# Kernel tuning notes

Hardware: AMD Instinct MI355X
Metric: run time of the kernel (lower is better)

The kernel has to match this reference:

```python
import math
import jax, jax.numpy as jnp
import numpy as np

N, E, D, B, S, H = 16384, 196608, 256, 256, 64, 8
DH = D // H
BN_INV = 1.0 / math.sqrt(1.0 + 1e-5)  # eval-mode BN: mean=0, var=1, eps=1e-5
LOG2 = math.log(2.0)


def _mlp(x, w1, b1, w2, b2):
    # Linear -> SiLU -> Linear
    return jax.nn.silu(x @ w1 + b1) @ w2 + b2


def _bn(x, g, b):
    # BatchNorm1d in eval mode with running_mean=0, running_var=1
    return x * (BN_INV * g) + b


def _graph_ln(x, g, b):
    # pyg LayerNorm(mode='graph') called with batch=None: normalize over all nodes+features
    mu = jnp.mean(x)
    xc = x - mu
    var = jnp.mean(xc * xc)
    return xc * jax.lax.rsqrt(var + 1e-5) * g + b


def _forward(x, edge_index, edge_attr,
             node_w1, node_b1, node_w2, node_b2,
             c_w1, c_b1, c_w2, c_b2,
             bn_e_g, bn_e_b, bn_h_g, bn_h_b,
             n1l_g, n1l_b, n1a_g, n1a_b, n2_g, n2_b,
             wq, bq, wk, bk, wv, bv, wo, bo,
             aff_w1, aff_b1, aff_w2, aff_b2,
             fn_g, fn_b, fc_w1, fc_b1, fc_w2, fc_b2):
    row, col = edge_index[0], edge_index[1]

    # ---- PotNetConvGate local branch ----
    # A, B, V, U MLPs (all take node features) computed with stacked weights [4,D,D]
    hid = jax.nn.silu(jnp.einsum('nd,kdf->knf', x, node_w1) + node_b1[:, None, :])
    node_out = jnp.einsum('knf,kfg->kng', hid, node_w2) + node_b2[:, None, :]
    h_A, h_B, h_V, h_U = node_out[0], node_out[1], node_out[2], node_out[3]
    e_C = _mlp(edge_attr, c_w1, c_b1, c_w2, c_b2)  # [E,D]

    score = jax.nn.relu(_bn(h_A[row] + h_B[col] + e_C, bn_e_g, bn_e_b))  # [E,D]
    e_new = edge_attr + score

    # pyg softmax over edges grouped by destination node (col), per channel
    m = jax.ops.segment_max(e_new, col, num_segments=N)        # [N,D]
    ex = jnp.exp(e_new - m[col])
    s = jax.ops.segment_sum(ex, col, num_segments=N)           # [N,D]
    gated = ex / (s[col] + 1e-16)

    msg = gated * (h_V[col] + e_new)
    aggr = jax.ops.segment_sum(msg, col, num_segments=N)       # [N,D]
    h_local = jax.nn.silu(x + _bn(h_U + aggr, bn_h_g, bn_h_b))
    # e_out = silu(e_new + edge_attr)  # edge output, not used downstream for node output
    h_local = _bn(h_local, n1l_g, n1l_b)  # norm1_local

    # ---- global Transformer branch (equal-size graphs -> dense reshape, full mask) ----
    hd = x.reshape(B, S, D)
    q = (hd @ wq + bq).reshape(B, S, H, DH).transpose(0, 2, 1, 3)
    k = (hd @ wk + bk).reshape(B, S, H, DH).transpose(0, 2, 1, 3)
    v = (hd @ wv + bv).reshape(B, S, H, DH).transpose(0, 2, 1, 3)
    att = jax.nn.softmax(jnp.einsum('bhqd,bhkd->bhqk', q, k) / math.sqrt(DH), axis=-1)
    o = jnp.einsum('bhqk,bhkd->bhqd', att, v).transpose(0, 2, 1, 3).reshape(B, S, D)
    h_attn = (o @ wo + bo).reshape(N, D)

    h_attn = _bn(h_attn + x, n1a_g, n1a_b)  # norm1_attn
    t = jax.nn.gelu(h_attn @ aff_w1 + aff_b1, approximate=False) @ aff_w2 + aff_b2
    h_attn = _graph_ln(t + x, fn_g, fn_b)   # feed_norm

    # ---- fuse branches (mean over stacked outputs) ----
    h_new = (h_local + h_attn) * 0.5

    # ---- _ff_block: fc = Linear -> ShiftedSoftplus -> Linear ----
    ssp = jax.nn.softplus(h_new @ fc_w1 + fc_b1) - LOG2
    out = ssp @ fc_w2 + fc_b2
    return _bn(out + h_new, n2_g, n2_b)  # norm2


def setup_inputs():
    key = jax.random.key(0)
    ks = iter(jax.random.split(key, 64))
    sc = 1.0 / math.sqrt(D)
    def w(shape):
        return jax.random.normal(next(ks), shape, jnp.float32) * sc
    z = lambda *s: jnp.zeros(s, jnp.float32)
    o = lambda *s: jnp.ones(s, jnp.float32)
    return {
        'x': jax.random.normal(next(ks), (N, D), jnp.float32),
        'edge_index': jax.random.randint(next(ks), (2, E), 0, N, jnp.int32),
        'edge_attr': jax.random.normal(next(ks), (E, D), jnp.float32),
        'node_w1': w((4, D, D)), 'node_b1': z(4, D),
        'node_w2': w((4, D, D)), 'node_b2': z(4, D),
        'c_w1': w((D, D)), 'c_b1': z(D), 'c_w2': w((D, D)), 'c_b2': z(D),
        'bn_e_g': o(D), 'bn_e_b': z(D), 'bn_h_g': o(D), 'bn_h_b': z(D),
        'n1l_g': o(D), 'n1l_b': z(D), 'n1a_g': o(D), 'n1a_b': z(D),
        'n2_g': o(D), 'n2_b': z(D),
        'wq': w((D, D)), 'bq': z(D), 'wk': w((D, D)), 'bk': z(D),
        'wv': w((D, D)), 'bv': z(D), 'wo': w((D, D)), 'bo': z(D),
        'aff_w1': w((D, 2 * D)), 'aff_b1': z(2 * D),
        'aff_w2': w((2 * D, D)), 'aff_b2': z(D),
        'fn_g': o(D), 'fn_b': z(D),
        'fc_w1': w((D, 2 * D)), 'fc_b1': z(2 * D),
        'fc_w2': w((2 * D, D)), 'fc_b2': z(D),
    }


def reference(x, edge_index, edge_attr,
              node_w1, node_b1, node_w2, node_b2,
              c_w1, c_b1, c_w2, c_b2,
              bn_e_g, bn_e_b, bn_h_g, bn_h_b,
              n1l_g, n1l_b, n1a_g, n1a_b, n2_g, n2_b,
              wq, bq, wk, bk, wv, bv, wo, bo,
              aff_w1, aff_b1, aff_w2, aff_b2,
              fn_g, fn_b, fc_w1, fc_b1, fc_w2, fc_b2):
    return _forward(x, edge_index, edge_attr,
                    node_w1, node_b1, node_w2, node_b2,
                    c_w1, c_b1, c_w2, c_b2,
                    bn_e_g, bn_e_b, bn_h_g, bn_h_b,
                    n1l_g, n1l_b, n1a_g, n1a_b, n2_g, n2_b,
                    wq, bq, wk, bk, wv, bv, wo, bo,
                    aff_w1, aff_b1, aff_w2, aff_b2,
                    fn_g, fn_b, fc_w1, fc_b1, fc_w2, fc_b2)
```

## Files before the change

kernel.cpp:

```cpp
#include <hip/hip_runtime.h>
#include <hip/hip_bf16.h>
#include <stdint.h>

#define NN 16384
#define NE 196608
#define DD 256
#define ND 4194304
#define ECH 65536
#define BNINV 0.9999950000374997f
#define LOG2F_ 0.6931471805599453f

typedef __attribute__((ext_vector_type(8))) short short8v;
typedef __attribute__((ext_vector_type(4))) float float4v;

__device__ __forceinline__ float b2f(__hip_bfloat16 v) { return __bfloat162float(v); }
__device__ __forceinline__ __hip_bfloat16 f2b(float v) { return __float2bfloat16(v); }

__device__ __forceinline__ void gl_lds16(const __hip_bfloat16* g, __hip_bfloat16* l) {
  __builtin_amdgcn_global_load_lds((const __attribute__((address_space(1))) void*)g,
                                   (__attribute__((address_space(3))) void*)l, 16, 0, 0);
}

__device__ __forceinline__ float rdf(const void* p, size_t i, int fl) {
  return fl ? b2f(((const __hip_bfloat16*)p)[i]) : ((const float*)p)[i];
}

#define OFF_WT    0ul
#define OFF_PB    2883584ul
#define OFF_XB    2899968ul
#define OFF_HIDE  11288576ul
#define OFF_HNEWB 44843008ul
#define OFF_HN    53231616ul
#define OFF_HL    86786048ul
#define OFF_EN    120340480ul
#define OFF_QKV   120340480ul
#define OFF_O     170672128ul
#define OFF_HATTN 179060736ul
#define OFF_U     187449344ul
#define OFF_HNEW  204226560ul
#define OFF_TAIL  221003776ul

#define PB_NB1   0
#define PB_NB2   1024
#define PB_CB1   2048
#define PB_CB2   2304
#define PB_QKVB  2560
#define PB_BO    3328
#define PB_AB1   3584
#define PB_AB2   4096
#define PB_FB1   4352
#define PB_FB2   4864
#define PB_BNEG  5120
#define PB_BNEB  5376
#define PB_BNHG  5632
#define PB_BNHB  5888
#define PB_N1LG  6144
#define PB_N1LB  6400
#define PB_N1AG  6656
#define PB_N1AB  6912
#define PB_N2G   7168
#define PB_N2B   7424
#define PB_FNG   7680
#define PB_FNB   7936

__global__ void probe_kernel(const uint32_t* bneg_raw, int* flag) {
  if (threadIdx.x == 0 && blockIdx.x == 0)
    *flag = (bneg_raw[0] == 0x3F803F80u) ? 1 : 0;
}

struct PJobs {
  const void* src[24];
  int off[24];
  int len[24];
};

__global__ void canon_params(PJobs jb, __hip_bfloat16* PB, const int* flagp) {
  const int fl = *flagp;
  const int j = blockIdx.x;
  const void* src = jb.src[j];
  const int off = jb.off[j], len = jb.len[j];
  for (int i = threadIdx.x; i < len; i += 256) PB[off + i] = f2b(rdf(src, i, fl));
}

__global__ void canon_x(const void* x, __hip_bfloat16* XB, const int* flagp) {
  const int fl = *flagp;
  const size_t i = (size_t)blockIdx.x * 256 + threadIdx.x;
  XB[i] = f2b(rdf(x, i, fl));
}

struct TJobsF {
  const void* src[18];
  __hip_bfloat16* dst[18];
  int R[18];
  int C[18];
  int RB[18];
};

__global__ void transpose_rb(TJobsF jb, const int* flagp) {
  __shared__ __hip_bfloat16 tile[32][33];
  const int fl = *flagp;
  const int j = blockIdx.z;
  const int R = jb.R[j], C = jb.C[j], RB = jb.RB[j];
  const int c0 = blockIdx.x * 32, r0 = blockIdx.y * 32;
  if (c0 >= C || r0 >= R) return;
  const void* src = jb.src[j];
  __hip_bfloat16* dst = jb.dst[j];
  const int tx = threadIdx.x, ty = threadIdx.y;
#pragma unroll
  for (int i = 0; i < 4; ++i)
    tile[ty + i * 8][tx] = f2b(rdf(src, (size_t)(RB + r0 + ty + i * 8) * C + c0 + tx, fl));
  __syncthreads();
#pragma unroll
  for (int i = 0; i < 4; ++i)
    dst[(long)(c0 + ty + i * 8) * R + r0 + tx] = tile[tx][ty + i * 8];
}

__global__ void prep_kernel(int* counts, double* stats) {
  const int i = blockIdx.x * blockDim.x + threadIdx.x;
  if (i < NN) counts[i] = 0;
  if (i == 0) counts[NN] = 0;
  if (i < 2) stats[i] = 0.0;
}

template <int ACT, int RES, int BNM, int OUTBF, int ASRC, int DUALOUT>
__global__ __launch_bounds__(256) void gemm_bt(
    const void* __restrict__ Avp, const __hip_bfloat16* __restrict__ Wt,
    const __hip_bfloat16* __restrict__ bias, const void* __restrict__ Res,
    const __hip_bfloat16* __restrict__ bng, const __hip_bfloat16* __restrict__ bnb,
    void* __restrict__ Cout, const int* __restrict__ flagp,
    int M, int N, int K, long boff, long az, long wz, long bz, long cz) {
  __shared__ __align__(16) __hip_bfloat16 sA[128 * 32];
  __shared__ __align__(16) __hip_bfloat16 sB[128 * 32];
  const int fl = (ASRC || DUALOUT) ? *flagp : 1;
  const int z = blockIdx.z;
  const long aoff = boff + (long)z * az;
  const __hip_bfloat16* Ab = (const __hip_bfloat16*)Avp + aoff;
  const float* Af = (const float*)Avp + aoff;
  Wt += (long)z * wz;
  bias += (long)z * bz;
  const long coff = (long)z * cz;
  const int tid = threadIdx.x;
  const int lane = tid & 63;
  const int wid = tid >> 6;
  const int wm = wid >> 1, wn = wid & 1;
  const int l16 = lane & 15, lq = lane >> 4;
  const long am0 = (long)blockIdx.y * 128;
  const long bn0 = (long)blockIdx.x * 128;

  float4v acc[4][4] = {};

  const int nK = K >> 5;
  for (int kb = 0; kb < nK; ++kb) {
    if (ASRC == 1 && fl == 0) {
#pragma unroll
      for (int r = 0; r < 2; ++r) {
        const int c = tid + r * 256;
        const float* ap = Af + (am0 + (c >> 2)) * K + kb * 32 + (c & 3) * 8;
        const float4v f0 = *(const float4v*)ap;
        const float4v f1 = *(const float4v*)(ap + 4);
        short8v s;
#pragma unroll
        for (int i = 0; i < 4; ++i) {
          __hip_bfloat16 h0 = f2b(f0[i]), h1 = f2b(f1[i]);
          s[i] = *(short*)&h0;
          s[4 + i] = *(short*)&h1;
        }
        ((short8v*)sA)[c] = s;
        gl_lds16(Wt + (bn0 + (c >> 2)) * K + kb * 32 + (c & 3) * 8, sB + c * 8);
      }
    } else {
#pragma unroll
      for (int r = 0; r < 2; ++r) {
        const int c = tid + r * 256;
        gl_lds16(Ab + (am0 + (c >> 2)) * K + kb * 32 + (c & 3) * 8, sA + c * 8);
        gl_lds16(Wt + (bn0 + (c >> 2)) * K + kb * 32 + (c & 3) * 8, sB + c * 8);
      }
    }
    __syncthreads();
    const short* pA = (const short*)sA;
    const short* pB = (const short*)sB;
    short8v af[4], bv_[4];
#pragma unroll
    for (int mi = 0; mi < 4; ++mi)
      af[mi] = *(const short8v*)(pA + (wm * 64 + mi * 16 + l16) * 32 + lq * 8);
#pragma unroll
    for (int ni = 0; ni < 4; ++ni)
      bv_[ni] = *(const short8v*)(pB + (wn * 64 + ni * 16 + l16) * 32 + lq * 8);
#pragma unroll
    for (int mi = 0; mi < 4; ++mi)
#pragma unroll
      for (int ni = 0; ni < 4; ++ni)
        acc[mi][ni] =
            __builtin_amdgcn_mfma_f32_16x16x32_bf16(af[mi], bv_[ni], acc[mi][ni], 0, 0, 0);
    __syncthreads();
  }

  const __hip_bfloat16* Rb = (const __hip_bfloat16*)Res;
  const float* Rf = (const float*)Res;
#pragma unroll
  for (int mi = 0; mi < 4; ++mi) {
#pragma unroll
    for (int ni = 0; ni < 4; ++ni) {
#pragma unroll
      for (int r = 0; r < 4; ++r) {
        const long row = am0 + wm * 64 + mi * 16 + lq * 4 + r;
        const long col = bn0 + wn * 64 + ni * 16 + l16;
        float v = acc[mi][ni][r] + b2f(bias[col]);
        if (ACT == 1) v = v / (1.f + expf(-v));
        else if (ACT == 2) v = 0.5f * v * (1.f + erff(v * 0.7071067811865476f));
        else if (ACT == 3) v = (v > 15.f ? v : log1pf(expf(v))) - LOG2F_;
        if (RES == 1) v += b2f(Rb[row * N + col]);
        else if (RES == 2) v += Rf[row * N + col];
        if (BNM) v = v * (BNINV * b2f(bng[col])) + b2f(bnb[col]);
        if (DUALOUT) {
          if (fl) ((__hip_bfloat16*)Cout)[coff + row * N + col] = f2b(v);
          else ((float*)Cout)[coff + row * N + col] = v;
        } else if (OUTBF) {
          ((__hip_bfloat16*)Cout)[coff + row * N + col] = f2b(v);
        } else {
          ((float*)Cout)[coff + row * N + col] = v;
        }
      }
    }
  }
}

__global__ __launch_bounds__(256) void gemm_edge2(
    const __hip_bfloat16* __restrict__ A, const __hip_bfloat16* __restrict__ Wt,
    const __hip_bfloat16* __restrict__ bias, const int* __restrict__ ei,
    const void* __restrict__ eattr, const __hip_bfloat16* __restrict__ HA,
    __hip_bfloat16* __restrict__ EN, const __hip_bfloat16* __restrict__ PB,
    const int* __restrict__ flagp, long ebase) {
  __shared__ __align__(16) __hip_bfloat16 sA[128 * 32];
  __shared__ __align__(16) __hip_bfloat16 sB[128 * 32];
  const int fl = *flagp;
  const int tid = threadIdx.x;
  const int lane = tid & 63;
  const int wid = tid >> 6;
  const int wm = wid >> 1, wn = wid & 1;
  const int l16 = lane & 15, lq = lane >> 4;
  const long am0 = (long)blockIdx.y * 128;
  const long bn0 = (long)blockIdx.x * 128;
  const __hip_bfloat16* HB = HA + (size_t)ND;

  float4v acc[4][4] = {};

  const int K = DD;
  for (int kb = 0; kb < (K >> 5); ++kb) {
#pragma unroll
    for (int r = 0; r < 2; ++r) {
      const int c = tid + r * 256;
      gl_lds16(A + (am0 + (c >> 2)) * K + kb * 32 + (c & 3) * 8, sA + c * 8);
      gl_lds16(Wt + (bn0 + (c >> 2)) * K + kb * 32 + (c & 3) * 8, sB + c * 8);
    }
    __syncthreads();
    const short* pA = (const short*)sA;
    const short* pB = (const short*)sB;
    short8v af[4], bv_[4];
#pragma unroll
    for (int mi = 0; mi < 4; ++mi)
      af[mi] = *(const short8v*)(pA + (wm * 64 + mi * 16 + l16) * 32 + lq * 8);
#pragma unroll
    for (int ni = 0; ni < 4; ++ni)
      bv_[ni] = *(const short8v*)(pB + (wn * 64 + ni * 16 + l16) * 32 + lq * 8);
#pragma unroll
    for (int mi = 0; mi < 4; ++mi)
#pragma unroll
      for (int ni = 0; ni < 4; ++ni)
        acc[mi][ni] =
            __builtin_amdgcn_mfma_f32_16x16x32_bf16(af[mi], bv_[ni], acc[mi][ni], 0, 0, 0);
    __syncthreads();
  }

#pragma unroll
  for (int mi = 0; mi < 4; ++mi) {
#pragma unroll
    for (int r = 0; r < 4; ++r) {
      const long row = am0 + wm * 64 + mi * 16 + lq * 4 + r;
      const long ge = ebase + row;
      const int rr = ei[ge];
      const int cc = ei[NE + ge];
#pragma unroll
      for (int ni = 0; ni < 4; ++ni) {
        const long col = bn0 + wn * 64 + ni * 16 + l16;
        float v = acc[mi][ni][r] + b2f(bias[col]);
        v += b2f(HA[(size_t)rr * DD + col]) + b2f(HB[(size_t)cc * DD + col]);
        v = v * (BNINV * b2f(PB[PB_BNEG + col])) + b2f(PB[PB_BNEB + col]);
        v = fmaxf(v, 0.f);
        v += rdf(eattr, (size_t)ge * DD + col, fl);
        EN[(size_t)ge * DD + col] = f2b(v);
      }
    }
  }
}

__global__ void count_kernel(const int* __restrict__ ei, int* __restrict__ counts) {
  const int e = blockIdx.x * 256 + threadIdx.x;
  if (e < NE) atomicAdd(&counts[ei[NE + e]], 1);
}

__global__ __launch_bounds__(1024) void scan_kernel(int* __restrict__ counts,
                                                    int* __restrict__ cursor) {
  __shared__ int part[1024];
  const int t = threadIdx.x;
  const int base = t * 16;
  int ss = 0;
#pragma unroll
  for (int i = 0; i < 16; ++i) ss += counts[base + i];
  part[t] = ss;
  __syncthreads();
  for (int off = 1; off < 1024; off <<= 1) {
    int v = (t >= off) ? part[t - off] : 0;
    __syncthreads();
    part[t] += v;
    __syncthreads();
  }
  int run = part[t] - ss;
  for (int i = 0; i < 16; ++i) {
    const int cv = counts[base + i];
    counts[base + i] = run;
    cursor[base + i] = run;
    run += cv;
  }
  if (t == 1023) counts[NN] = run;
}

__global__ void scatter_kernel(const int* __restrict__ ei, int* __restrict__ cursor,
                               int* __restrict__ eids) {
  const int e = blockIdx.x * 256 + threadIdx.x;
  if (e < NE) {
    const int p = atomicAdd(&cursor[ei[NE + e]], 1);
    eids[p] = e;
  }
}

__global__ __launch_bounds__(256) void segment_kernel(
    const int* __restrict__ offs, const int* __restrict__ eids,
    const __hip_bfloat16* __restrict__ EN, const __hip_bfloat16* __restrict__ hV,
    const __hip_bfloat16* __restrict__ hU, const __hip_bfloat16* __restrict__ XB,
    const __hip_bfloat16* __restrict__ PB, float* __restrict__ hlocal) {
  __shared__ int sEid[256];
  const int n = blockIdx.x;
  const int d = threadIdx.x;
  const int beg = offs[n], end = offs[n + 1];
  float sa = 0.f, sb = 0.f;
  for (int base = beg; base < end; base += 256) {
    const int cnt = min(256, end - base);
    __syncthreads();
    if (threadIdx.x < cnt) sEid[threadIdx.x] = eids[base + threadIdx.x];
    __syncthreads();
    for (int i = 0; i < cnt; ++i) {
      const float v = b2f(EN[(size_t)sEid[i] * DD + d]);
      const float e = expf(v);
      sa += e;
      sb += e * v;
    }
  }
  const float hv = b2f(hV[(size_t)n * DD + d]);
  const float ag = (hv * sa + sb) / (sa + 1e-16f);
  const float t1 =
      (b2f(hU[(size_t)n * DD + d]) + ag) * (BNINV * b2f(PB[PB_BNHG + d])) + b2f(PB[PB_BNHB + d]);
  float s1 = b2f(XB[(size_t)n * DD + d]) + t1;
  s1 = s1 / (1.f + expf(-s1));
  s1 = s1 * (BNINV * b2f(PB[PB_N1LG + d])) + b2f(PB[PB_N1LB + d]);
  hlocal[(size_t)n * DD + d] = s1;
}

__global__ __launch_bounds__(256) void attn_kernel(const float* __restrict__ QKV,
                                                   __hip_bfloat16* __restrict__ O) {
  __shared__ float sq[64][33], sk[64][33], sv[64][33];
  __shared__ float sp[64][65];
  const int bh = blockIdx.x;
  const int b = bh >> 3, h = bh & 7;
  const int tid = threadIdx.x;
  const float* Q = QKV;
  const float* Kp = QKV + (size_t)ND;
  const float* Vp = QKV + 2 * (size_t)ND;
#pragma unroll
  for (int j = 0; j < 8; ++j) {
    const int idx = j * 256 + tid;
    const int s = idx >> 5, dh = idx & 31;
    const size_t ga = ((size_t)(b * 64 + s)) * DD + h * 32 + dh;
    sq[s][dh] = Q[ga];
    sk[s][dh] = Kp[ga];
    sv[s][dh] = Vp[ga];
  }
  __syncthreads();
  const int row = tid >> 2, l4 = tid & 3;
  float qr[32];
#pragma unroll
  for (int d = 0; d < 32; ++d) qr[d] = sq[row][d];
  float sc[16];
  float mx = -1e30f;
#pragma unroll
  for (int jj = 0; jj < 16; ++jj) {
    const int j = l4 * 16 + jj;
    float dot = 0.f;
#pragma unroll
    for (int d = 0; d < 32; ++d) dot += qr[d] * sk[j][d];
    dot *= 0.17677669529663687f;
    sc[jj] = dot;
    mx = fmaxf(mx, dot);
  }
  mx = fmaxf(mx, __shfl_xor(mx, 1));
  mx = fmaxf(mx, __shfl_xor(mx, 2));
  float se = 0.f;
#pragma unroll
  for (int jj = 0; jj < 16; ++jj) {
    sc[jj] = expf(sc[jj] - mx);
    se += sc[jj];
  }
  se += __shfl_xor(se, 1);
  se += __shfl_xor(se, 2);
  const float inv = 1.f / se;
#pragma unroll
  for (int jj = 0; jj < 16; ++jj) sp[row][l4 * 16 + jj] = sc[jj] * inv;
  __syncthreads();
#pragma unroll
  for (int k8 = 0; k8 < 8; ++k8) {
    const int dh = l4 * 8 + k8;
    float acc = 0.f;
#pragma unroll
    for (int j = 0; j < 64; ++j) acc += sp[row][j] * sv[j][dh];
    O[((size_t)(b * 64 + row)) * DD + h * 32 + dh] = f2b(acc);
  }
}

__global__ __launch_bounds__(256) void stats_kernel(const float* __restrict__ U,
                                                    double* __restrict__ st) {
  double s = 0.0, s2 = 0.0;
  for (size_t i = (size_t)blockIdx.x * 256 + threadIdx.x; i < (size_t)ND;
       i += (size_t)gridDim.x * 256) {
    const double v = (double)U[i];
    s += v;
    s2 += v * v;
  }
  for (int o = 32; o > 0; o >>= 1) {
    s += __shfl_down(s, o);
    s2 += __shfl_down(s2, o);
  }
  __shared__ double wred[4][2];
  const int lane = threadIdx.x & 63, w = threadIdx.x >> 6;
  if (lane == 0) {
    wred[w][0] = s;
    wred[w][1] = s2;
  }
  __syncthreads();
  if (threadIdx.x == 0) {
    double a = 0, bb = 0;
    for (int i = 0; i < 4; ++i) {
      a += wred[i][0];
      bb += wred[i][1];
    }
    atomicAdd(&st[0], a);
    atomicAdd(&st[1], bb);
  }
}

__global__ void finalize_stats(double* st) {
  if (threadIdx.x == 0 && blockIdx.x == 0) {
    const double mu = st[0] / (double)ND;
    const double var = st[1] / (double)ND - mu * mu;
    float* f = (float*)(st + 2);
    f[0] = (float)mu;
    f[1] = (float)(1.0 / sqrt(var + 1e-5));
  }
}

__global__ void hnew_kernel(const float* __restrict__ U, const float* __restrict__ hlocal,
                            const double* __restrict__ st, const __hip_bfloat16* __restrict__ PB,
                            float* __restrict__ HNEW, __hip_bfloat16* __restrict__ HNEWB) {
  const size_t i = (size_t)blockIdx.x * 256 + threadIdx.x;
  const float* f = (const float*)(st + 2);
  const float mu = f[0], rs = f[1];
  const int d = (int)(i & 255);
  const float ha = (U[i] - mu) * rs * b2f(PB[PB_FNG + d]) + b2f(PB[PB_FNB + d]);
  const float hn = 0.5f * (hlocal[i] + ha);
  HNEW[i] = hn;
  HNEWB[i] = f2b(hn);
}

extern "C" void kernel_launch(void* const* d_in, const int* in_sizes, int n_in, void* d_out,
                              int out_size, void* d_ws, size_t ws_size, hipStream_t stream) {
  (void)in_sizes; (void)n_in; (void)out_size; (void)ws_size;
  const void* x = d_in[0];
  const int* ei = (const int*)d_in[1];
  const void* eattr = d_in[2];

  uint8_t* ws = (uint8_t*)d_ws;
  __hip_bfloat16* WT = (__hip_bfloat16*)(ws + OFF_WT);
  __hip_bfloat16* PB = (__hip_bfloat16*)(ws + OFF_PB);
  __hip_bfloat16* XB = (__hip_bfloat16*)(ws + OFF_XB);
  __hip_bfloat16* HIDE = (__hip_bfloat16*)(ws + OFF_HIDE);
  __hip_bfloat16* HNEWB = (__hip_bfloat16*)(ws + OFF_HNEWB);
  __hip_bfloat16* HN = (__hip_bfloat16*)(ws + OFF_HN);
  float* HL = (float*)(ws + OFF_HL);
  __hip_bfloat16* EN = (__hip_bfloat16*)(ws + OFF_EN);
  float* QKV = (float*)(ws + OFF_QKV);
  __hip_bfloat16* O = (__hip_bfloat16*)(ws + OFF_O);
  __hip_bfloat16* HATTN = (__hip_bfloat16*)(ws + OFF_HATTN);
  float* U = (float*)(ws + OFF_U);
  float* HNEW = (float*)(ws + OFF_HNEW);
  uint8_t* tail = ws + OFF_TAIL;
  int* counts = (int*)tail;
  int* cursor = (int*)(tail + 66048ul);
  int* eids = (int*)(tail + 132096ul);
  double* stats = (double*)(tail + 918528ul);
  int* flag = (int*)(tail + 918592ul);

  probe_kernel<<<1, 64, 0, stream>>>((const uint32_t*)d_in[11], flag);

  PJobs pj;
  {
    const int srcidx[24] = {4, 6, 8, 10, 22, 24, 26, 28, 30, 32, 36, 38,
                            11, 12, 13, 14, 15, 16, 17, 18, 19, 20, 33, 34};
    const int dstoff[24] = {PB_NB1, PB_NB2, PB_CB1, PB_CB2, PB_QKVB, PB_QKVB + 256,
                            PB_QKVB + 512, PB_BO, PB_AB1, PB_AB2, PB_FB1, PB_FB2,
                            PB_BNEG, PB_BNEB, PB_BNHG, PB_BNHB, PB_N1LG, PB_N1LB,
                            PB_N1AG, PB_N1AB, PB_N2G, PB_N2B, PB_FNG, PB_FNB};
    const int lens[24] = {1024, 1024, 256, 256, 256, 256, 256, 256, 512, 256, 512, 256,
                          256, 256, 256, 256, 256, 256, 256, 256, 256, 256, 256, 256};
    for (int i = 0; i < 24; ++i) {
      pj.src[i] = d_in[srcidx[i]];
      pj.off[i] = dstoff[i];
      pj.len[i] = lens[i];
    }
  }
  canon_params<<<24, 256, 0, stream>>>(pj, PB, flag);
  canon_x<<<NN, 256, 0, stream>>>(x, XB, flag);

  TJobsF jf;
  for (int j = 0; j < 4; ++j) {
    jf.src[j] = d_in[3]; jf.dst[j] = WT + j * 65536;
    jf.R[j] = 256; jf.C[j] = 256; jf.RB[j] = j * 256;
    jf.src[4 + j] = d_in[5]; jf.dst[4 + j] = WT + 262144 + j * 65536;
    jf.R[4 + j] = 256; jf.C[4 + j] = 256; jf.RB[4 + j] = j * 256;
  }
  {
    const int widx[10] = {7, 9, 21, 23, 25, 27, 29, 31, 35, 37};
    const long wdst[10] = {524288, 589824, 655360, 720896, 786432, 851968,
                           917504, 1048576, 1179648, 1310720};
    const int wR[10] = {256, 256, 256, 256, 256, 256, 256, 512, 256, 512};
    const int wC[10] = {256, 256, 256, 256, 256, 256, 512, 256, 512, 256};
    for (int j = 0; j < 10; ++j) {
      jf.src[8 + j] = d_in[widx[j]]; jf.dst[8 + j] = WT + wdst[j];
      jf.R[8 + j] = wR[j]; jf.C[8 + j] = wC[j]; jf.RB[8 + j] = 0;
    }
  }
  transpose_rb<<<dim3(16, 16, 18), dim3(32, 8), 0, stream>>>(jf, flag);

  prep_kernel<<<64, 256, 0, stream>>>(counts, stats);

  count_kernel<<<768, 256, 0, stream>>>(ei, counts);
  scan_kernel<<<1, 1024, 0, stream>>>(counts, cursor);
  scatter_kernel<<<768, 256, 0, stream>>>(ei, cursor, eids);

  gemm_bt<1, 0, 0, 1, 0, 0><<<dim3(2, 128, 4), 256, 0, stream>>>(
      XB, WT, PB + PB_NB1, nullptr, nullptr, nullptr, HIDE, flag,
      NN, DD, DD, 0, 0, 65536, 256, ND);
  gemm_bt<0, 0, 0, 1, 0, 0><<<dim3(2, 128, 4), 256, 0, stream>>>(
      HIDE, WT + 262144, PB + PB_NB2, nullptr, nullptr, nullptr, HN, flag,
      NN, DD, DD, 0, ND, 65536, 256, ND);

  for (int ch = 0; ch < 3; ++ch) {
    const long eo = (long)ch * ECH * DD;
    gemm_bt<1, 0, 0, 1, 1, 0><<<dim3(2, 512, 1), 256, 0, stream>>>(
        eattr, WT + 524288, PB + PB_CB1, nullptr, nullptr, nullptr, HIDE, flag,
        ECH, DD, DD, eo, 0, 0, 0, 0);
    gemm_edge2<<<dim3(2, 512, 1), 256, 0, stream>>>(
        HIDE, WT + 589824, PB + PB_CB2, ei, eattr, HN, EN, PB, flag, (long)ch * ECH);
  }

  segment_kernel<<<NN, 256, 0, stream>>>(counts, eids, EN, HN + 2 * (size_t)ND,
                                         HN + 3 * (size_t)ND, XB, PB, HL);

  gemm_bt<0, 0, 0, 0, 0, 0><<<dim3(2, 128, 3), 256, 0, stream>>>(
      XB, WT + 655360, PB + PB_QKVB, nullptr, nullptr, nullptr, QKV, flag,
      NN, DD, DD, 0, 0, 65536, 256, ND);
  attn_kernel<<<2048, 256, 0, stream>>>(QKV, O);
  gemm_bt<0, 1, 1, 1, 0, 0><<<dim3(2, 128, 1), 256, 0, stream>>>(
      O, WT + 851968, PB + PB_BO, XB, PB + PB_N1AG, PB + PB_N1AB, HATTN, flag,
      NN, DD, DD, 0, 0, 0, 0, 0);

  gemm_bt<2, 0, 0, 1, 0, 0><<<dim3(4, 128, 1), 256, 0, stream>>>(
      HATTN, WT + 917504, PB + PB_AB1, nullptr, nullptr, nullptr, HIDE, flag,
      NN, 512, DD, 0, 0, 0, 0, 0);
  gemm_bt<0, 1, 0, 0, 0, 0><<<dim3(2, 128, 1), 256, 0, stream>>>(
      HIDE, WT + 1048576, PB + PB_AB2, XB, nullptr, nullptr, U, flag,
      NN, DD, 512, 0, 0, 0, 0, 0);

  stats_kernel<<<1024, 256, 0, stream>>>(U, stats);
  finalize_stats<<<1, 64, 0, stream>>>(stats);
  hnew_kernel<<<NN, 256, 0, stream>>>(U, HL, stats, PB, HNEW, HNEWB);

  gemm_bt<3, 0, 0, 1, 0, 0><<<dim3(4, 128, 1), 256, 0, stream>>>(
      HNEWB, WT + 1179648, PB + PB_FB1, nullptr, nullptr, nullptr, HIDE, flag,
      NN, 512, DD, 0, 0, 0, 0, 0);
  gemm_bt<0, 2, 1, 1, 0, 1><<<dim3(2, 128, 1), 256, 0, stream>>>(
      HIDE, WT + 1310720, PB + PB_FB2, HNEW, PB + PB_N2G, PB + PB_N2B, d_out, flag,
      NN, DD, 512, 0, 0, 0, 0, 0);
}
```

Baseline: 1.036 ms.

## Store intermediates in bf16, merge edge chunks, and drop probe and prep kernels

QKV, hlocal, U and HNEW intermediates move from fp32 to bf16, which halves their memory traffic. The three edge-chunk GEMM pairs become one launch over all edges with a dedicated hidden buffer. The probe and prep kernels are removed: every kernel now reads the dtype flag inline, and canon_x zeroes counts and stats. The cost is lower precision in the residual paths, including the final residual into the output, and a larger workspace.

```diff
diff --git a/kernel.cpp b/kernel.cpp
--- a/kernel.cpp
+++ b/kernel.cpp
@@ -6,7 +6,6 @@
 #define NE 196608
 #define DD 256
 #define ND 4194304
-#define ECH 65536
 #define BNINV 0.9999950000374997f
 #define LOG2F_ 0.6931471805599453f
 
@@ -21,24 +20,26 @@
                                    (__attribute__((address_space(3))) void*)l, 16, 0, 0);
 }
 
+__device__ __forceinline__ int dtfl(const uint32_t* dt) { return dt[0] == 0x3F803F80u ? 1 : 0; }
+
 __device__ __forceinline__ float rdf(const void* p, size_t i, int fl) {
   return fl ? b2f(((const __hip_bfloat16*)p)[i]) : ((const float*)p)[i];
 }
 
-#define OFF_WT    0ul
-#define OFF_PB    2883584ul
-#define OFF_XB    2899968ul
-#define OFF_HIDE  11288576ul
-#define OFF_HNEWB 44843008ul
-#define OFF_HN    53231616ul
-#define OFF_HL    86786048ul
-#define OFF_EN    120340480ul
-#define OFF_QKV   120340480ul
-#define OFF_O     170672128ul
-#define OFF_HATTN 179060736ul
-#define OFF_U     187449344ul
-#define OFF_HNEW  204226560ul
-#define OFF_TAIL  221003776ul
+#define OFF_WT     0ul
+#define OFF_PB     2883584ul
+#define OFF_XB     2899968ul
+#define OFF_HN     11288576ul
+#define OFF_HL     44843008ul
+#define OFF_HNEWB  53231616ul
+#define OFF_HIDE   61620224ul
+#define OFF_EN     95174656ul
+#define OFF_HIDE_E 195837952ul
+#define OFF_QKVB   296501248ul
+#define OFF_OB     321667072ul
+#define OFF_HATTN  330055680ul
+#define OFF_UB     338444288ul
+#define OFF_TAIL   346832896ul
 
 #define PB_NB1   0
 #define PB_NB2   1024
@@ -63,29 +64,28 @@
 #define PB_FNG   7680
 #define PB_FNB   7936
 
-__global__ void probe_kernel(const uint32_t* bneg_raw, int* flag) {
-  if (threadIdx.x == 0 && blockIdx.x == 0)
-    *flag = (bneg_raw[0] == 0x3F803F80u) ? 1 : 0;
-}
-
 struct PJobs {
   const void* src[24];
   int off[24];
   int len[24];
 };
 
-__global__ void canon_params(PJobs jb, __hip_bfloat16* PB, const int* flagp) {
-  const int fl = *flagp;
+__global__ void canon_params(PJobs jb, __hip_bfloat16* PB, const uint32_t* dt) {
+  const int fl = dtfl(dt);
   const int j = blockIdx.x;
   const void* src = jb.src[j];
   const int off = jb.off[j], len = jb.len[j];
   for (int i = threadIdx.x; i < len; i += 256) PB[off + i] = f2b(rdf(src, i, fl));
 }
 
-__global__ void canon_x(const void* x, __hip_bfloat16* XB, const int* flagp) {
-  const int fl = *flagp;
+__global__ void canon_x(const void* x, __hip_bfloat16* XB, const uint32_t* dt,
+                        int* counts, double* stats) {
+  const int fl = dtfl(dt);
   const size_t i = (size_t)blockIdx.x * 256 + threadIdx.x;
   XB[i] = f2b(rdf(x, i, fl));
+  if (i < NN) counts[i] = 0;
+  if (i == 0) counts[NN] = 0;
+  if (i < 2) stats[i] = 0.0;
 }
 
 struct TJobsF {
@@ -96,9 +96,9 @@
   int RB[18];
 };
 
-__global__ void transpose_rb(TJobsF jb, const int* flagp) {
+__global__ void transpose_rb(TJobsF jb, const uint32_t* dt) {
   __shared__ __hip_bfloat16 tile[32][33];
-  const int fl = *flagp;
+  const int fl = dtfl(dt);
   const int j = blockIdx.z;
   const int R = jb.R[j], C = jb.C[j], RB = jb.RB[j];
   const int c0 = blockIdx.x * 32, r0 = blockIdx.y * 32;
@@ -115,25 +115,18 @@
     dst[(long)(c0 + ty + i * 8) * R + r0 + tx] = tile[tx][ty + i * 8];
 }
 
-__global__ void prep_kernel(int* counts, double* stats) {
-  const int i = blockIdx.x * blockDim.x + threadIdx.x;
-  if (i < NN) counts[i] = 0;
-  if (i == 0) counts[NN] = 0;
-  if (i < 2) stats[i] = 0.0;
-}
-
-template <int ACT, int RES, int BNM, int OUTBF, int ASRC, int DUALOUT>
+template <int ACT, int RES, int BNM, int ASRC, int DUALOUT>
 __global__ __launch_bounds__(256) void gemm_bt(
     const void* __restrict__ Avp, const __hip_bfloat16* __restrict__ Wt,
-    const __hip_bfloat16* __restrict__ bias, const void* __restrict__ Res,
+    const __hip_bfloat16* __restrict__ bias, const __hip_bfloat16* __restrict__ Res,
     const __hip_bfloat16* __restrict__ bng, const __hip_bfloat16* __restrict__ bnb,
-    void* __restrict__ Cout, const int* __restrict__ flagp,
-    int M, int N, int K, long boff, long az, long wz, long bz, long cz) {
+    void* __restrict__ Cout, const uint32_t* __restrict__ dt,
+    int M, int N, int K, long az, long wz, long bz, long cz) {
   __shared__ __align__(16) __hip_bfloat16 sA[128 * 32];
   __shared__ __align__(16) __hip_bfloat16 sB[128 * 32];
-  const int fl = (ASRC || DUALOUT) ? *flagp : 1;
+  const int fl = (ASRC || DUALOUT) ? dtfl(dt) : 1;
   const int z = blockIdx.z;
-  const long aoff = boff + (long)z * az;
+  const long aoff = (long)z * az;
   const __hip_bfloat16* Ab = (const __hip_bfloat16*)Avp + aoff;
   const float* Af = (const float*)Avp + aoff;
   Wt += (long)z * wz;
@@ -195,8 +188,6 @@
     __syncthreads();
   }
 
-  const __hip_bfloat16* Rb = (const __hip_bfloat16*)Res;
-  const float* Rf = (const float*)Res;
 #pragma unroll
   for (int mi = 0; mi < 4; ++mi) {
 #pragma unroll
@@ -209,16 +200,13 @@
         if (ACT == 1) v = v / (1.f + expf(-v));
         else if (ACT == 2) v = 0.5f * v * (1.f + erff(v * 0.7071067811865476f));
         else if (ACT == 3) v = (v > 15.f ? v : log1pf(expf(v))) - LOG2F_;
-        if (RES == 1) v += b2f(Rb[row * N + col]);
-        else if (RES == 2) v += Rf[row * N + col];
+        if (RES == 1) v += b2f(Res[row * N + col]);
         if (BNM) v = v * (BNINV * b2f(bng[col])) + b2f(bnb[col]);
         if (DUALOUT) {
           if (fl) ((__hip_bfloat16*)Cout)[coff + row * N + col] = f2b(v);
           else ((float*)Cout)[coff + row * N + col] = v;
-        } else if (OUTBF) {
+        } else {
           ((__hip_bfloat16*)Cout)[coff + row * N + col] = f2b(v);
-        } else {
-          ((float*)Cout)[coff + row * N + col] = v;
         }
       }
     }
@@ -230,10 +218,10 @@
     const __hip_bfloat16* __restrict__ bias, const int* __restrict__ ei,
     const void* __restrict__ eattr, const __hip_bfloat16* __restrict__ HA,
     __hip_bfloat16* __restrict__ EN, const __hip_bfloat16* __restrict__ PB,
-    const int* __restrict__ flagp, long ebase) {
+    const uint32_t* __restrict__ dt) {
   __shared__ __align__(16) __hip_bfloat16 sA[128 * 32];
   __shared__ __align__(16) __hip_bfloat16 sB[128 * 32];
-  const int fl = *flagp;
+  const int fl = dtfl(dt);
   const int tid = threadIdx.x;
   const int lane = tid & 63;
   const int wid = tid >> 6;
@@ -276,8 +264,7 @@
   for (int mi = 0; mi < 4; ++mi) {
 #pragma unroll
     for (int r = 0; r < 4; ++r) {
-      const long row = am0 + wm * 64 + mi * 16 + lq * 4 + r;
-      const long ge = ebase + row;
+      const long ge = am0 + wm * 64 + mi * 16 + lq * 4 + r;
       const int rr = ei[ge];
       const int cc = ei[NE + ge];
 #pragma unroll
@@ -338,7 +325,7 @@
     const int* __restrict__ offs, const int* __restrict__ eids,
     const __hip_bfloat16* __restrict__ EN, const __hip_bfloat16* __restrict__ hV,
     const __hip_bfloat16* __restrict__ hU, const __hip_bfloat16* __restrict__ XB,
-    const __hip_bfloat16* __restrict__ PB, float* __restrict__ hlocal) {
+    const __hip_bfloat16* __restrict__ PB, __hip_bfloat16* __restrict__ hlocal) {
   __shared__ int sEid[256];
   const int n = blockIdx.x;
   const int d = threadIdx.x;
@@ -363,27 +350,27 @@
   float s1 = b2f(XB[(size_t)n * DD + d]) + t1;
   s1 = s1 / (1.f + expf(-s1));
   s1 = s1 * (BNINV * b2f(PB[PB_N1LG + d])) + b2f(PB[PB_N1LB + d]);
-  hlocal[(size_t)n * DD + d] = s1;
-}
-
-__global__ __launch_bounds__(256) void attn_kernel(const float* __restrict__ QKV,
+  hlocal[(size_t)n * DD + d] = f2b(s1);
+}
+
+__global__ __launch_bounds__(256) void attn_kernel(const __hip_bfloat16* __restrict__ QKV,
                                                    __hip_bfloat16* __restrict__ O) {
   __shared__ float sq[64][33], sk[64][33], sv[64][33];
   __shared__ float sp[64][65];
   const int bh = blockIdx.x;
   const int b = bh >> 3, h = bh & 7;
   const int tid = threadIdx.x;
-  const float* Q = QKV;
-  const float* Kp = QKV + (size_t)ND;
-  const float* Vp = QKV + 2 * (size_t)ND;
+  const __hip_bfloat16* Q = QKV;
+  const __hip_bfloat16* Kp = QKV + (size_t)ND;
+  const __hip_bfloat16* Vp = QKV + 2 * (size_t)ND;
 #pragma unroll
   for (int j = 0; j < 8; ++j) {
     const int idx = j * 256 + tid;
     const int s = idx >> 5, dh = idx & 31;
     const size_t ga = ((size_t)(b * 64 + s)) * DD + h * 32 + dh;
-    sq[s][dh] = Q[ga];
-    sk[s][dh] = Kp[ga];
-    sv[s][dh] = Vp[ga];
+    sq[s][dh] = b2f(Q[ga]);
+    sk[s][dh] = b2f(Kp[ga]);
+    sv[s][dh] = b2f(Vp[ga]);
   }
   __syncthreads();
   const int row = tid >> 2, l4 = tid & 3;
@@ -426,12 +413,12 @@
   }
 }
 
-__global__ __launch_bounds__(256) void stats_kernel(const float* __restrict__ U,
+__global__ __launch_bounds__(256) void stats_kernel(const __hip_bfloat16* __restrict__ U,
                                                     double* __restrict__ st) {
   double s = 0.0, s2 = 0.0;
   for (size_t i = (size_t)blockIdx.x * 256 + threadIdx.x; i < (size_t)ND;
        i += (size_t)gridDim.x * 256) {
-    const double v = (double)U[i];
+    const double v = (double)b2f(U[i]);
     s += v;
     s2 += v * v;
   }
@@ -467,17 +454,16 @@
   }
 }
 
-__global__ void hnew_kernel(const float* __restrict__ U, const float* __restrict__ hlocal,
+__global__ void hnew_kernel(const __hip_bfloat16* __restrict__ U,
+                            const __hip_bfloat16* __restrict__ hlocal,
                             const double* __restrict__ st, const __hip_bfloat16* __restrict__ PB,
-                            float* __restrict__ HNEW, __hip_bfloat16* __restrict__ HNEWB) {
+                            __hip_bfloat16* __restrict__ HNEWB) {
   const size_t i = (size_t)blockIdx.x * 256 + threadIdx.x;
   const float* f = (const float*)(st + 2);
   const float mu = f[0], rs = f[1];
   const int d = (int)(i & 255);
-  const float ha = (U[i] - mu) * rs * b2f(PB[PB_FNG + d]) + b2f(PB[PB_FNB + d]);
-  const float hn = 0.5f * (hlocal[i] + ha);
-  HNEW[i] = hn;
-  HNEWB[i] = f2b(hn);
+  const float ha = (b2f(U[i]) - mu) * rs * b2f(PB[PB_FNG + d]) + b2f(PB[PB_FNB + d]);
+  HNEWB[i] = f2b(0.5f * (b2f(hlocal[i]) + ha));
 }
 
 extern "C" void kernel_launch(void* const* d_in, const int* in_sizes, int n_in, void* d_out,
@@ -486,29 +472,27 @@
   const void* x = d_in[0];
   const int* ei = (const int*)d_in[1];
   const void* eattr = d_in[2];
+  const uint32_t* dt = (const uint32_t*)d_in[11];
 
   uint8_t* ws = (uint8_t*)d_ws;
   __hip_bfloat16* WT = (__hip_bfloat16*)(ws + OFF_WT);
   __hip_bfloat16* PB = (__hip_bfloat16*)(ws + OFF_PB);
   __hip_bfloat16* XB = (__hip_bfloat16*)(ws + OFF_XB);
+  __hip_bfloat16* HN = (__hip_bfloat16*)(ws + OFF_HN);
+  __hip_bfloat16* HL = (__hip_bfloat16*)(ws + OFF_HL);
+  __hip_bfloat16* HNEWB = (__hip_bfloat16*)(ws + OFF_HNEWB);
   __hip_bfloat16* HIDE = (__hip_bfloat16*)(ws + OFF_HIDE);
-  __hip_bfloat16* HNEWB = (__hip_bfloat16*)(ws + OFF_HNEWB);
-  __hip_bfloat16* HN = (__hip_bfloat16*)(ws + OFF_HN);
-  float* HL = (float*)(ws + OFF_HL);
   __hip_bfloat16* EN = (__hip_bfloat16*)(ws + OFF_EN);
-  float* QKV = (float*)(ws + OFF_QKV);
-  __hip_bfloat16* O = (__hip_bfloat16*)(ws + OFF_O);
+  __hip_bfloat16* HIDE_E = (__hip_bfloat16*)(ws + OFF_HIDE_E);
+  __hip_bfloat16* QKVB = (__hip_bfloat16*)(ws + OFF_QKVB);
+  __hip_bfloat16* OB = (__hip_bfloat16*)(ws + OFF_OB);
   __hip_bfloat16* HATTN = (__hip_bfloat16*)(ws + OFF_HATTN);
-  float* U = (float*)(ws + OFF_U);
-  float* HNEW = (float*)(ws + OFF_HNEW);
+  __hip_bfloat16* UB = (__hip_bfloat16*)(ws + OFF_UB);
   uint8_t* tail = ws + OFF_TAIL;
   int* counts = (int*)tail;
   int* cursor = (int*)(tail + 66048ul);
   int* eids = (int*)(tail + 132096ul);
   double* stats = (double*)(tail + 918528ul);
-  int* flag = (int*)(tail + 918592ul);
-
-  probe_kernel<<<1, 64, 0, stream>>>((const uint32_t*)d_in[11], flag);
 
   PJobs pj;
   {
@@ -526,8 +510,8 @@
       pj.len[i] = lens[i];
     }
   }
-  canon_params<<<24, 256, 0, stream>>>(pj, PB, flag);
-  canon_x<<<NN, 256, 0, stream>>>(x, XB, flag);
+  canon_params<<<24, 256, 0, stream>>>(pj, PB, dt);
+  canon_x<<<NN, 256, 0, stream>>>(x, XB, dt, counts, stats);
 
   TJobsF jf;
   for (int j = 0; j < 4; ++j) {
@@ -547,56 +531,51 @@
       jf.R[8 + j] = wR[j]; jf.C[8 + j] = wC[j]; jf.RB[8 + j] = 0;
     }
   }
-  transpose_rb<<<dim3(16, 16, 18), dim3(32, 8), 0, stream>>>(jf, flag);
-
-  prep_kernel<<<64, 256, 0, stream>>>(counts, stats);
+  transpose_rb<<<dim3(16, 16, 18), dim3(32, 8), 0, stream>>>(jf, dt);
 
   count_kernel<<<768, 256, 0, stream>>>(ei, counts);
   scan_kernel<<<1, 1024, 0, stream>>>(counts, cursor);
   scatter_kernel<<<768, 256, 0, stream>>>(ei, cursor, eids);
 
-  gemm_bt<1, 0, 0, 1, 0, 0><<<dim3(2, 128, 4), 256, 0, stream>>>(
-      XB, WT, PB + PB_NB1, nullptr, nullptr, nullptr, HIDE, flag,
-      NN, DD, DD, 0, 0, 65536, 256, ND);
-  gemm_bt<0, 0, 0, 1, 0, 0><<<dim3(2, 128, 4), 256, 0, stream>>>(
-      HIDE, WT + 262144, PB + PB_NB2, nullptr, nullptr, nullptr, HN, flag,
-      NN, DD, DD, 0, ND, 65536, 256, ND);
-
-  for (int ch = 0; ch < 3; ++ch) {
-    const long eo = (long)ch * ECH * DD;
-    gemm_bt<1, 0, 0, 1, 1, 0><<<dim3(2, 512, 1), 256, 0, stream>>>(
-        eattr, WT + 524288, PB + PB_CB1, nullptr, nullptr, nullptr, HIDE, flag,
-        ECH, DD, DD, eo, 0, 0, 0, 0);
-    gemm_edge2<<<dim3(2, 512, 1), 256, 0, stream>>>(
-        HIDE, WT + 589824, PB + PB_CB2, ei, eattr, HN, EN, PB, flag, (long)ch * ECH);
-  }
+  gemm_bt<1, 0, 0, 0, 0><<<dim3(2, 128, 4), 256, 0, stream>>>(
+      XB, WT, PB + PB_NB1, nullptr, nullptr, nullptr, HIDE, dt,
+      NN, DD, DD, 0, 65536, 256, ND);
+  gemm_bt<0, 0, 0, 0, 0><<<dim3(2, 128, 4), 256, 0, stream>>>(
+      HIDE, WT + 262144, PB + PB_NB2, nullptr, nullptr, nullptr, HN, dt,
+      NN, DD, DD, ND, 65536, 256, ND);
+
+  gemm_bt<1, 0, 0, 1, 0><<<dim3(2, 1536, 1), 256, 0, stream>>>(
+      eattr, WT + 524288, PB + PB_CB1, nullptr, nullptr, nullptr, HIDE_E, dt,
+      NE, DD, DD, 0, 0, 0, 0);
+  gemm_edge2<<<dim3(2, 1536, 1), 256, 0, stream>>>(
+      HIDE_E, WT + 589824, PB + PB_CB2, ei, eattr, HN, EN, PB, dt);
 
   segment_kernel<<<NN, 256, 0, stream>>>(counts, eids, EN, HN + 2 * (size_t)ND,
                                          HN + 3 * (size_t)ND, XB, PB, HL);
 
-  gemm_bt<0, 0, 0, 0, 0, 0><<<dim3(2, 128, 3), 256, 0, stream>>>(
-      XB, WT + 655360, PB + PB_QKVB, nullptr, nullptr, nullptr, QKV, flag,
-      NN, DD, DD, 0, 0, 65536, 256, ND);
-  attn_kernel<<<2048, 256, 0, stream>>>(QKV, O);
-  gemm_bt<0, 1, 1, 1, 0, 0><<<dim3(2, 128, 1), 256, 0, stream>>>(
-      O, WT + 851968, PB + PB_BO, XB, PB + PB_N1AG, PB + PB_N1AB, HATTN, flag,
-      NN, DD, DD, 0, 0, 0, 0, 0);
-
-  gemm_bt<2, 0, 0, 1, 0, 0><<<dim3(4, 128, 1), 256, 0, stream>>>(
-      HATTN, WT + 917504, PB + PB_AB1, nullptr, nullptr, nullptr, HIDE, flag,
-      NN, 512, DD, 0, 0, 0, 0, 0);
-  gemm_bt<0, 1, 0, 0, 0, 0><<<dim3(2, 128, 1), 256, 0, stream>>>(
-      HIDE, WT + 1048576, PB + PB_AB2, XB, nullptr, nullptr, U, flag,
-      NN, DD, 512, 0, 0, 0, 0, 0);
-
-  stats_kernel<<<1024, 256, 0, stream>>>(U, stats);
+  gemm_bt<0, 0, 0, 0, 0><<<dim3(2, 128, 3), 256, 0, stream>>>(
+      XB, WT + 655360, PB + PB_QKVB, nullptr, nullptr, nullptr, QKVB, dt,
+      NN, DD, DD, 0, 65536, 256, ND);
+  attn_kernel<<<2048, 256, 0, stream>>>(QKVB, OB);
+  gemm_bt<0, 1, 1, 0, 0><<<dim3(2, 128, 1), 256, 0, stream>>>(
+      OB, WT + 851968, PB + PB_BO, XB, PB + PB_N1AG, PB + PB_N1AB, HATTN, dt,
+      NN, DD, DD, 0, 0, 0, 0);
+
+  gemm_bt<2, 0, 0, 0, 0><<<dim3(4, 128, 1), 256, 0, stream>>>(
+      HATTN, WT + 917504, PB + PB_AB1, nullptr, nullptr, nullptr, HIDE, dt,
+      NN, 512, DD, 0, 0, 0, 0);
+  gemm_bt<0, 1, 0, 0, 0><<<dim3(2, 128, 1), 256, 0, stream>>>(
+      HIDE, WT + 1048576, PB + PB_AB2, XB, nullptr, nullptr, UB, dt,
+      NN, DD, 512, 0, 0, 0, 0);
+
+  stats_kernel<<<1024, 256, 0, stream>>>(UB, stats);
   finalize_stats<<<1, 64, 0, stream>>>(stats);
-  hnew_kernel<<<NN, 256, 0, stream>>>(U, HL, stats, PB, HNEW, HNEWB);
-
-  gemm_bt<3, 0, 0, 1, 0, 0><<<dim3(4, 128, 1), 256, 0, stream>>>(
-      HNEWB, WT + 1179648, PB + PB_FB1, nullptr, nullptr, nullptr, HIDE, flag,
-      NN, 512, DD, 0, 0, 0, 0, 0);
-  gemm_bt<0, 2, 1, 1, 0, 1><<<dim3(2, 128, 1), 256, 0, stream>>>(
-      HIDE, WT + 1310720, PB + PB_FB2, HNEW, PB + PB_N2G, PB + PB_N2B, d_out, flag,
-      NN, DD, 512, 0, 0, 0, 0, 0);
-}
+  hnew_kernel<<<NN, 256, 0, stream>>>(UB, HL, stats, PB, HNEWB);
+
+  gemm_bt<3, 0, 0, 0, 0><<<dim3(4, 128, 1), 256, 0, stream>>>(
+      HNEWB, WT + 1179648, PB + PB_FB1, nullptr, nullptr, nullptr, HIDE, dt,
+      NN, 512, DD, 0, 0, 0, 0);
+  gemm_bt<0, 1, 1, 0, 1><<<dim3(2, 128, 1), 256, 0, stream>>>(
+      HIDE, WT + 1310720, PB + PB_FB2, HNEWB, PB + PB_N2G, PB + PB_N2B, d_out, dt,
+      NN, DD, 512, 0, 0, 0, 0);
+}
```

Result: slower. 1.277 ms (+23.3%).
